# Kernel tuning notes

Measured on AMD Instinct MI355X. Metric: run time of the kernel, lower is better.

## Reference

```python
import math
import jax, jax.numpy as jnp
import numpy as np

HIDDEN = 1024
HEADS = 16
HEAD = HIDDEN // HEADS
BUCKET = 32
MAXPOS = 512
REL = 2 * BUCKET - 1
EPS = 1e-7
L, B = 512, 16
STD = math.sqrt(2.0 / (5.0 * HIDDEN))


def _ln(x, g=None, b=None):
    m = x.mean(-1, keepdims=True)
    v = ((x - m) ** 2).mean(-1, keepdims=True)
    y = (x - m) * jax.lax.rsqrt(v + EPS)
    return y if g is None else y * g + b


def _bucket_indices(n):
    # DeBERTa-style log bucket relative positions, shifted to [0, 2*BUCKET-2]
    r = jnp.arange(n)[:, None] - jnp.arange(n)[None, :]
    mid = BUCKET // 2
    abs_pos = jnp.where((r < mid) & (r > -mid), mid - 1,
                        jnp.clip(jnp.abs(r), None, MAXPOS - 1))
    log_pos = jnp.ceil(jnp.log(abs_pos.astype(jnp.float32) / mid)
                       / math.log((MAXPOS - 1) / mid) * (mid - 1)).astype(jnp.int32) + mid
    bucket_pos = jnp.where(abs_pos <= mid, r, log_pos * jnp.sign(r))
    return (BUCKET - 1 + bucket_pos).astype(jnp.int32)


def setup_inputs() -> dict:
    key = jax.random.key(0)
    ks = jax.random.split(key, 8)
    return {
        'hidden_states': jax.random.normal(ks[0], (L, B, HIDDEN), jnp.float32),
        'attention_mask': jax.random.randint(ks[1], (B, 1, 1, L), 0, 2).astype(bool),
        'relative_embedding': jax.random.normal(ks[2], (REL, HIDDEN), jnp.float32),
        'wqk': jax.random.normal(ks[3], (2 * HIDDEN, HIDDEN), jnp.float32) * STD,
        'bqk': jnp.zeros((2 * HIDDEN,), jnp.float32),
        'wv': jax.random.normal(ks[4], (HIDDEN, HIDDEN), jnp.float32) * STD,
        'bv': jnp.zeros((HIDDEN,), jnp.float32),
        'wo': jax.random.normal(ks[5], (HIDDEN, HIDDEN), jnp.float32) * STD,
        'bo': jnp.zeros((HIDDEN,), jnp.float32),
        'ln_g': jnp.ones((HIDDEN,), jnp.float32),
        'ln_b': jnp.zeros((HIDDEN,), jnp.float32),
    }


def reference(hidden_states, attention_mask, relative_embedding,
              wqk, bqk, wv, bv, wo, bo, ln_g, ln_b):
    Lq, Bq, D = hidden_states.shape
    scale = 1.0 / math.sqrt(3 * HEAD)
    h = _ln(hidden_states)                                 # pre LN, no affine
    q, k = jnp.split(h @ wqk.T + bqk, 2, axis=-1)
    v = h @ wv.T + bv
    qpos, kpos = jnp.split(relative_embedding @ wqk.T + bqk, 2, axis=-1)
    qpos = qpos.reshape(REL, HEADS, HEAD)
    kpos = kpos.reshape(REL, HEADS, HEAD)
    # (L,B,D) -> (B,H,L,hd)
    qh = q.reshape(Lq, Bq, HEADS, HEAD).transpose(1, 2, 0, 3)
    kh = k.reshape(Lq, Bq, HEADS, HEAD).transpose(1, 2, 0, 3)
    vh = v.reshape(Lq, Bq, HEADS, HEAD).transpose(1, 2, 0, 3)
    scores = jnp.einsum('bhqd,bhkd->bhqk', qh, kh) * scale       # c2c
    qp = jnp.einsum('bhqd,khd->bhqk', qh, kpos) * scale          # c2p (k over buckets)
    pk = jnp.einsum('bhkd,qhd->bhqk', kh, qpos) * scale          # p2c (q over buckets)
    idx = jnp.broadcast_to(_bucket_indices(Lq), (Bq, HEADS, Lq, Lq))
    scores = scores + jnp.take_along_axis(qp, idx, axis=-1) \
                    + jnp.take_along_axis(pk, idx, axis=-2)
    # masked softmax: mask==True -> -inf before softmax, 0 after
    probs = jax.nn.softmax(jnp.where(attention_mask, -1e9, scores), axis=-1)
    probs = jnp.where(attention_mask, 0.0, probs)
    ctx = jnp.einsum('bhqk,bhkd->bhqd', probs, vh)
    ctx = ctx.transpose(2, 0, 1, 3).reshape(Lq, Bq, D)           # (L,B,D)
    out = ctx @ wo.T + bo
    return _ln(out, ln_g, ln_b)
```

## Files before the change

### kernel.cpp

```cpp
#include <hip/hip_runtime.h>
#include <hip/hip_bf16.h>

#define HID 1024
#define HEADS 16
#define HEAD 64
#define RELN 63
#define SEQ 512
#define BATCH 16
#define NROWS (SEQ*BATCH)
#define MEXT 8320
#define NQKV 3072
#define LNEPS 1e-7f
#define SCALE2 (0.07216878364870323f * 1.4426950408889634f)

typedef __attribute__((ext_vector_type(4))) float  f32x4;
typedef __attribute__((ext_vector_type(8))) short  s16x8;
typedef __attribute__((ext_vector_type(4))) ushort u16x4;

static __device__ __forceinline__ ushort f2bf(float f) {
  union { float f; unsigned u; } v; v.f = f;
  unsigned r = v.u + 0x7fffu + ((v.u >> 16) & 1u);
  return (ushort)(r >> 16);
}
static __device__ __forceinline__ float bf2f(ushort u) {
  union { unsigned u; float f; } v; v.u = ((unsigned)u) << 16;
  return v.f;
}

__global__ void k_prep(const void* mask_raw, const float* bqk, const float* bv,
                       ushort* mask01, int* idx_tab, float* bcat) {
  __shared__ int s_isbool;
  int tid = threadIdx.x;
  if (tid == 0) s_isbool = 0;
  __syncthreads();
  const unsigned* mu = (const unsigned*)mask_raw;
  int bad = 0;
  for (int i = tid; i < 2048; i += 256) if (mu[i] > 1u) bad = 1;
  if (bad) s_isbool = 1;
  __syncthreads();
  int isbool = s_isbool;
  const unsigned char* m8 = (const unsigned char*)mask_raw;
  const int* m32 = (const int*)mask_raw;
  for (int i = tid; i < BATCH*SEQ; i += 256) {
    int m = isbool ? (int)m8[i] : m32[i];
    mask01[i] = m ? 1 : 0;
  }
  for (int i = tid; i < 1023; i += 256) {
    int r = i - 511;
    int a = r < 0 ? -r : r;
    int absp = (a < 16) ? 15 : (a < 511 ? a : 511);
    int idx;
    if (absp <= 16) idx = 31 + r;
    else {
      float v = logf((float)absp / 16.0f) / logf(511.0f / 16.0f) * 15.0f;
      int lp = (int)ceilf(v) + 16;
      idx = 31 + (r > 0 ? lp : -lp);
    }
    idx_tab[i] = idx;
  }
  for (int i = tid; i < 2048; i += 256) bcat[i] = bqk[i];
  for (int i = tid; i < 1024; i += 256) bcat[2048 + i] = bv[i];
}

__global__ __launch_bounds__(256) void k_convert(const float* wqk, const float* wv, const float* wo,
                                                 ushort* wcat, ushort* wo_b) {
  int c = blockIdx.x * 256 + threadIdx.x;
  f32x4 x; ushort* dst;
  if (c < 524288)      { x = *(const f32x4*)(wqk + (size_t)c * 4);            dst = wcat + (size_t)c * 4; }
  else if (c < 786432) { x = *(const f32x4*)(wv  + (size_t)(c - 524288) * 4); dst = wcat + (size_t)c * 4; }
  else                 { x = *(const f32x4*)(wo  + (size_t)(c - 786432) * 4); dst = wo_b + (size_t)(c - 786432) * 4; }
  u16x4 o = { f2bf(x[0]), f2bf(x[1]), f2bf(x[2]), f2bf(x[3]) };
  *(u16x4*)dst = o;
}

__global__ __launch_bounds__(256) void k_ln1(const float* hid, const float* rel, ushort* h_ext) {
  int row = blockIdx.x, tid = threadIdx.x;
  __shared__ float red[8];
  if (row < NROWS) {
    const float* src = hid + (size_t)row * HID;
    f32x4 x = *(const f32x4*)(src + tid * 4);
    float s = x[0] + x[1] + x[2] + x[3];
    #pragma unroll
    for (int m = 1; m < 64; m <<= 1) s += __shfl_xor(s, m);
    if ((tid & 63) == 0) red[tid >> 6] = s;
    __syncthreads();
    float mean = (red[0] + red[1] + red[2] + red[3]) * (1.0f / HID);
    float d0 = x[0] - mean, d1 = x[1] - mean, d2 = x[2] - mean, d3 = x[3] - mean;
    float sq = d0*d0 + d1*d1 + d2*d2 + d3*d3;
    #pragma unroll
    for (int m = 1; m < 64; m <<= 1) sq += __shfl_xor(sq, m);
    __syncthreads();
    if ((tid & 63) == 0) red[4 + (tid >> 6)] = sq;
    __syncthreads();
    float var = (red[4] + red[5] + red[6] + red[7]) * (1.0f / HID);
    float rs = rsqrtf(var + LNEPS);
    u16x4 o = { f2bf(d0*rs), f2bf(d1*rs), f2bf(d2*rs), f2bf(d3*rs) };
    *(u16x4*)(h_ext + (size_t)row * HID + tid * 4) = o;
  } else if (row < NROWS + RELN) {
    const float* src = rel + (size_t)(row - NROWS) * HID;
    f32x4 x = *(const f32x4*)(src + tid * 4);
    u16x4 o = { f2bf(x[0]), f2bf(x[1]), f2bf(x[2]), f2bf(x[3]) };
    *(u16x4*)(h_ext + (size_t)row * HID + tid * 4) = o;
  } else {
    u16x4 z = { 0, 0, 0, 0 };
    *(u16x4*)(h_ext + (size_t)row * HID + tid * 4) = z;
  }
}

__global__ __launch_bounds__(512) void k_gemm256(const ushort* A, const ushort* Bw, const float* bias,
                                                 ushort* Cb, int M, int N, int K) {
  __shared__ char smem[49152];
  char* As = smem;
  char* Bs = smem + 32768;
  int tid = threadIdx.x, lane = tid & 63, w = tid >> 6;
  int nbn = N >> 7;
  int per = gridDim.x >> 3;
  int gl = (blockIdx.x & 7) * per + (blockIdx.x >> 3);
  int bm = gl / nbn, bn = gl % nbn;
  int wr = w >> 1, wc = w & 1;
  int g = lane >> 4, r = lane & 15;
  f32x4 acc[4][4] = {};
  for (int ko = 0; ko < K; ko += 64) {
    __syncthreads();
    #pragma unroll
    for (int c = 0; c < 4; ++c) {
      int chunk = c * 512 + tid;
      int row = chunk >> 3;
      int kbs = ((chunk & 7) << 4) ^ ((row & 7) << 4);
      int ar = bm * 256 + row; ar = ar < M ? ar : M - 1;
      const char* gA = (const char*)(A + (size_t)ar * K + ko) + kbs;
      __builtin_amdgcn_global_load_lds((const __attribute__((address_space(1))) void*)gA,
                                       (__attribute__((address_space(3))) void*)(As + c * 8192 + w * 1024),
                                       16, 0, 0);
    }
    #pragma unroll
    for (int c = 0; c < 2; ++c) {
      int chunk = c * 512 + tid;
      int row = chunk >> 3;
      int kbs = ((chunk & 7) << 4) ^ ((row & 7) << 4);
      const char* gB = (const char*)(Bw + (size_t)(bn * 128 + row) * K + ko) + kbs;
      __builtin_amdgcn_global_load_lds((const __attribute__((address_space(1))) void*)gB,
                                       (__attribute__((address_space(3))) void*)(Bs + c * 8192 + w * 1024),
                                       16, 0, 0);
    }
    __syncthreads();
    #pragma unroll
    for (int kk = 0; kk < 2; ++kk) {
      s16x8 af[4], bf[4];
      #pragma unroll
      for (int mt = 0; mt < 4; ++mt) {
        int row = wr * 64 + mt * 16 + r;
        int kb = (kk * 64 + g * 16) ^ ((row & 7) << 4);
        af[mt] = *(const s16x8*)(As + row * 128 + kb);
      }
      #pragma unroll
      for (int nt = 0; nt < 4; ++nt) {
        int row = wc * 64 + nt * 16 + r;
        int kb = (kk * 64 + g * 16) ^ ((row & 7) << 4);
        bf[nt] = *(const s16x8*)(Bs + row * 128 + kb);
      }
      #pragma unroll
      for (int mt = 0; mt < 4; ++mt)
        #pragma unroll
        for (int nt = 0; nt < 4; ++nt)
          acc[mt][nt] = __builtin_amdgcn_mfma_f32_16x16x32_bf16(af[mt], bf[nt], acc[mt][nt], 0, 0, 0);
    }
  }
  #pragma unroll
  for (int nt = 0; nt < 4; ++nt) {
    int col = bn * 128 + wc * 64 + nt * 16 + r;
    float bvv = bias[col];
    #pragma unroll
    for (int mt = 0; mt < 4; ++mt) {
      int row0 = bm * 256 + wr * 64 + mt * 16 + g * 4;
      #pragma unroll
      for (int i = 0; i < 4; ++i) {
        int row = row0 + i;
        if (row < M) Cb[(size_t)row * N + col] = f2bf(acc[mt][nt][i] + bvv);
      }
    }
  }
}

__global__ __launch_bounds__(256) void k_gemm_sk(const ushort* A, const ushort* Bw, const float* bias,
                                                 ushort* C0, ushort* C1) {
  const int N = 1024, K = 1024;
  __shared__ char smem[32768];
  char* As = smem;
  char* Bs = smem + 16384;
  int tid = threadIdx.x, lane = tid & 63, w = tid >> 6;
  int per = gridDim.x >> 3;
  int gl = (blockIdx.x & 7) * per + (blockIdx.x >> 3);
  int bn = gl & 7, ks = (gl >> 3) & 1, bm = gl >> 4;
  int wr = w >> 1, wc = w & 1;
  int g = lane >> 4, r = lane & 15;
  f32x4 acc[4][4] = {};
  for (int ko = ks * 512; ko < ks * 512 + 512; ko += 64) {
    __syncthreads();
    #pragma unroll
    for (int c = 0; c < 4; ++c) {
      int chunk = c * 256 + tid;
      int row = chunk >> 3;
      int kbs = ((chunk & 7) << 4) ^ ((row & 7) << 4);
      const char* gA = (const char*)(A + (size_t)(bm * 128 + row) * K + ko) + kbs;
      const char* gB = (const char*)(Bw + (size_t)(bn * 128 + row) * K + ko) + kbs;
      __builtin_amdgcn_global_load_lds((const __attribute__((address_space(1))) void*)gA,
                                       (__attribute__((address_space(3))) void*)(As + c * 4096 + w * 1024),
                                       16, 0, 0);
      __builtin_amdgcn_global_load_lds((const __attribute__((address_space(1))) void*)gB,
                                       (__attribute__((address_space(3))) void*)(Bs + c * 4096 + w * 1024),
                                       16, 0, 0);
    }
    __syncthreads();
    #pragma unroll
    for (int kk = 0; kk < 2; ++kk) {
      s16x8 af[4], bf[4];
      #pragma unroll
      for (int mt = 0; mt < 4; ++mt) {
        int row = wr * 64 + mt * 16 + r;
        int kb = (kk * 64 + g * 16) ^ ((row & 7) << 4);
        af[mt] = *(const s16x8*)(As + row * 128 + kb);
      }
      #pragma unroll
      for (int nt = 0; nt < 4; ++nt) {
        int row = wc * 64 + nt * 16 + r;
        int kb = (kk * 64 + g * 16) ^ ((row & 7) << 4);
        bf[nt] = *(const s16x8*)(Bs + row * 128 + kb);
      }
      #pragma unroll
      for (int mt = 0; mt < 4; ++mt)
        #pragma unroll
        for (int nt = 0; nt < 4; ++nt)
          acc[mt][nt] = __builtin_amdgcn_mfma_f32_16x16x32_bf16(af[mt], bf[nt], acc[mt][nt], 0, 0, 0);
    }
  }
  ushort* C = ks ? C1 : C0;
  #pragma unroll
  for (int nt = 0; nt < 4; ++nt) {
    int col = bn * 128 + wc * 64 + nt * 16 + r;
    float bvv = ks ? 0.0f : bias[col];
    #pragma unroll
    for (int mt = 0; mt < 4; ++mt) {
      int row0 = bm * 128 + wr * 64 + mt * 16 + g * 4;
      #pragma unroll
      for (int i = 0; i < 4; ++i)
        C[(size_t)(row0 + i) * N + col] = f2bf(acc[mt][nt][i] + bvv);
    }
  }
}

__global__ __launch_bounds__(256) void k_pos(const ushort* qkv, const ushort* mask01,
                                             ushort* qp, ushort* pk) {
  int bh = blockIdx.x;
  int b = bh >> 4, h = bh & 15;
  int tid = threadIdx.x, lane = tid & 63, w = tid >> 6;
  int g = lane >> 4, r = lane & 15;
  __shared__ ushort mb[512];
  for (int i = tid; i < 512; i += 256) mb[i] = mask01[b * SEQ + i];
  __syncthreads();
  s16x8 bkp[4][2], bqp[4][2];
  #pragma unroll
  for (int nt = 0; nt < 4; ++nt)
    #pragma unroll
    for (int kk = 0; kk < 2; ++kk) {
      size_t rowp = (size_t)(NROWS + nt * 16 + r);
      int colq = h * 64 + kk * 32 + g * 8;
      bqp[nt][kk] = *(const s16x8*)(qkv + rowp * NQKV + colq);
      bkp[nt][kk] = *(const s16x8*)(qkv + rowp * NQKV + 1024 + colq);
    }
  for (int cc = 0; cc < 8; ++cc) {
    int rowbase = cc * 64 + w * 16;
    s16x8 aq[2], ak[2];
    #pragma unroll
    for (int kk = 0; kk < 2; ++kk) {
      size_t rowq = (size_t)((rowbase + r) * 16 + b);
      int colq = h * 64 + kk * 32 + g * 8;
      aq[kk] = *(const s16x8*)(qkv + rowq * NQKV + colq);
      ak[kk] = *(const s16x8*)(qkv + rowq * NQKV + 1024 + colq);
    }
    f32x4 accq[4] = {}, acck[4] = {};
    #pragma unroll
    for (int kk = 0; kk < 2; ++kk)
      #pragma unroll
      for (int nt = 0; nt < 4; ++nt) {
        accq[nt] = __builtin_amdgcn_mfma_f32_16x16x32_bf16(aq[kk], bkp[nt][kk], accq[nt], 0, 0, 0);
        acck[nt] = __builtin_amdgcn_mfma_f32_16x16x32_bf16(ak[kk], bqp[nt][kk], acck[nt], 0, 0, 0);
      }
    #pragma unroll
    for (int nt = 0; nt < 4; ++nt)
      #pragma unroll
      for (int i = 0; i < 4; ++i) {
        int q = rowbase + g * 4 + i;
        int t = nt * 16 + r;
        float biasv = mb[q] ? -1e9f : 0.0f;
        qp[(size_t)bh * SEQ * 64 + q * 64 + t] = f2bf(accq[nt][i] * SCALE2);
        pk[(size_t)bh * SEQ * 64 + q * 64 + t] = f2bf(acck[nt][i] * SCALE2 + biasv);
      }
  }
}

__global__ __launch_bounds__(256) void k_vt(const ushort* qkv, ushort* vt, ushort* kc) {
  int bid = blockIdx.x;
  int bh = bid >> 3, lt = bid & 7;
  int b = bh >> 4, h = bh & 15;
  __shared__ ushort tile[64][72];
  int tid = threadIdx.x;
  #pragma unroll
  for (int c = 0; c < 2; ++c) {
    int e = (c * 256 + tid) * 8;
    int l = e >> 6, d0 = e & 63;
    size_t row = (size_t)((lt * 64 + l) * 16 + b);
    s16x8 kv = *(const s16x8*)(qkv + row * NQKV + 1024 + h * 64 + d0);
    #pragma unroll
    for (int j = 0; j < 8; ++j) kv[j] = (short)f2bf(bf2f((ushort)kv[j]) * SCALE2);
    *(s16x8*)(kc + ((size_t)bh * SEQ + lt * 64 + l) * 64 + d0) = kv;
    *(s16x8*)&tile[l][d0] = *(const s16x8*)(qkv + row * NQKV + 2048 + h * 64 + d0);
  }
  __syncthreads();
  #pragma unroll
  for (int c = 0; c < 2; ++c) {
    int e = (c * 256 + tid) * 8;
    int d = e >> 6, l0 = e & 63;
    ushort tmp[8];
    #pragma unroll
    for (int j = 0; j < 8; ++j) tmp[j] = tile[l0 + j][d];
    *(s16x8*)(vt + (size_t)(bh * 64 + d) * SEQ + lt * 64 + l0) = *(s16x8*)tmp;
  }
}

__global__ __launch_bounds__(512) void k_attn(const ushort* qkv, const ushort* qp_all, const ushort* pk_all,
                                              const ushort* kc, const ushort* vt,
                                              const int* idx_tab, ushort* ctx) {
  int bid = blockIdx.x;
  int slot = bid >> 3;
  int bh = (bid & 7) * 32 + (slot >> 1);
  int qh = slot & 1;
  int b = bh >> 4, h = bh & 15;
  int tid = threadIdx.x, lane = tid & 63, w = tid >> 6;
  int g = lane >> 4, r = lane & 15;

  __shared__ ushort pk_f[512][68];
  __shared__ ushort qp_s[256][68];
  __shared__ ushort p_s[8][16][68];
  __shared__ ushort idx_s[1024];

  const ushort* qpsrc = qp_all + (size_t)bh * SEQ * 64 + (size_t)qh * 256 * 64;
  const ushort* pksrc = pk_all + (size_t)bh * SEQ * 64;
  const char*   kcb   = (const char*)(kc + (size_t)bh * SEQ * 64);

  #pragma unroll
  for (int c = 0; c < 4; ++c) {
    int chunk = c * 512 + tid;
    int row = chunk >> 3, col8 = (chunk & 7) * 8;
    s16x8 v = *(const s16x8*)(qpsrc + (size_t)row * 64 + col8);
    u16x4 lo = { (ushort)v[0], (ushort)v[1], (ushort)v[2], (ushort)v[3] };
    u16x4 hi = { (ushort)v[4], (ushort)v[5], (ushort)v[6], (ushort)v[7] };
    *(u16x4*)&qp_s[row][col8] = lo;
    *(u16x4*)&qp_s[row][col8 + 4] = hi;
  }
  #pragma unroll
  for (int c = 0; c < 8; ++c) {
    int chunk = c * 512 + tid;
    int row = chunk >> 3, col8 = (chunk & 7) * 8;
    s16x8 v = *(const s16x8*)(pksrc + (size_t)row * 64 + col8);
    u16x4 lo = { (ushort)v[0], (ushort)v[1], (ushort)v[2], (ushort)v[3] };
    u16x4 hi = { (ushort)v[4], (ushort)v[5], (ushort)v[6], (ushort)v[7] };
    *(u16x4*)&pk_f[row][col8] = lo;
    *(u16x4*)&pk_f[row][col8 + 4] = hi;
  }
  for (int i = tid; i < 1023; i += 512) idx_s[i] = (ushort)idx_tab[i];
  s16x8 aq[2][2];
  #pragma unroll
  for (int qs = 0; qs < 2; ++qs)
    #pragma unroll
    for (int kk = 0; kk < 2; ++kk) {
      int qglob = qh * 256 + qs * 128 + w * 16 + r;
      aq[qs][kk] = *(const s16x8*)(qkv + ((size_t)qglob * 16 + b) * NQKV + h * 64 + kk * 32 + g * 8);
    }
  __syncthreads();

  float m_i[2] = { -3e38f, -3e38f }, l_i[2] = { 0.0f, 0.0f };
  f32x4 o_acc[2][4] = {};

  for (int kt = 0; kt < 8; ++kt) {
    s16x8 kf[4][2], vf[2][4];
    #pragma unroll
    for (int nt = 0; nt < 4; ++nt)
      #pragma unroll
      for (int kk = 0; kk < 2; ++kk)
        kf[nt][kk] = *(const s16x8*)(kcb + (size_t)(kt * 64 + nt * 16 + r) * 128 + kk * 64 + g * 16);
    #pragma unroll
    for (int kk = 0; kk < 2; ++kk)
      #pragma unroll
      for (int nt = 0; nt < 4; ++nt)
        vf[kk][nt] = *(const s16x8*)(vt + (size_t)(bh * 64 + nt * 16 + r) * SEQ + kt * 64 + kk * 32 + g * 8);

    #pragma unroll
    for (int qs = 0; qs < 2; ++qs) {
      f32x4 s[4];
      #pragma unroll
      for (int nt = 0; nt < 4; ++nt) {
        f32x4 a = {};
        #pragma unroll
        for (int kk = 0; kk < 2; ++kk)
          a = __builtin_amdgcn_mfma_f32_16x16x32_bf16(kf[nt][kk], aq[qs][kk], a, 0, 0, 0);
        s[nt] = a;
      }

      const ushort* qprow = &qp_s[qs * 128 + w * 16 + r][0];
      const int qg511 = qh * 256 + qs * 128 + w * 16 + r + 511;
      float m_loc = -3e38f;
      #pragma unroll
      for (int nt = 0; nt < 4; ++nt) {
        #pragma unroll
        for (int i = 0; i < 4; ++i) {
          int kg = kt * 64 + nt * 16 + g * 4 + i;
          int t = idx_s[qg511 - kg];
          float v = s[nt][i] + bf2f(qprow[t]) + bf2f(pk_f[kg][t]);
          s[nt][i] = v;
          m_loc = fmaxf(m_loc, v);
        }
      }

      float mx = fmaxf(m_loc, __shfl_xor(m_loc, 16));
      mx = fmaxf(mx, __shfl_xor(mx, 32));

      if (__any(mx > m_i[qs] + 8.0f)) {
        float mnew = fmaxf(m_i[qs], mx);
        float rs = exp2f(m_i[qs] - mnew);
        m_i[qs] = mnew;
        l_i[qs] *= rs;
        float rsb[4];
        #pragma unroll
        for (int i = 0; i < 4; ++i) rsb[i] = __shfl(rs, g * 4 + i);
        #pragma unroll
        for (int nt = 0; nt < 4; ++nt)
          #pragma unroll
          for (int i = 0; i < 4; ++i) o_acc[qs][nt][i] *= rsb[i];
      }

      float psum = 0.0f;
      #pragma unroll
      for (int nt = 0; nt < 4; ++nt) {
        u16x4 pk4;
        #pragma unroll
        for (int i = 0; i < 4; ++i) {
          float pe = exp2f(s[nt][i] - m_i[qs]);
          psum += pe;
          pk4[i] = f2bf(pe);
        }
        *(u16x4*)&p_s[w][r][nt * 16 + g * 4] = pk4;
      }
      psum += __shfl_xor(psum, 16);
      psum += __shfl_xor(psum, 32);
      l_i[qs] += psum;

      #pragma unroll
      for (int kk = 0; kk < 2; ++kk) {
        u16x4 lo = *(const u16x4*)&p_s[w][r][kk * 32 + g * 8];
        u16x4 hi = *(const u16x4*)&p_s[w][r][kk * 32 + g * 8 + 4];
        s16x8 pa = { (short)lo[0], (short)lo[1], (short)lo[2], (short)lo[3],
                     (short)hi[0], (short)hi[1], (short)hi[2], (short)hi[3] };
        #pragma unroll
        for (int nt = 0; nt < 4; ++nt)
          o_acc[qs][nt] = __builtin_amdgcn_mfma_f32_16x16x32_bf16(pa, vf[kk][nt], o_acc[qs][nt], 0, 0, 0);
      }
    }
  }

  #pragma unroll
  for (int qs = 0; qs < 2; ++qs) {
    float lb[4];
    #pragma unroll
    for (int i = 0; i < 4; ++i) lb[i] = __shfl(l_i[qs], g * 4 + i);
    #pragma unroll
    for (int i = 0; i < 4; ++i) {
      float inv = lb[i] > 0.0f ? 1.0f / lb[i] : 0.0f;
      int lq = qh * 256 + qs * 128 + w * 16 + g * 4 + i;
      size_t rowc = (size_t)(lq * 16 + b);
      #pragma unroll
      for (int nt = 0; nt < 4; ++nt)
        ctx[rowc * HID + h * 64 + nt * 16 + r] = f2bf(o_acc[qs][nt][i] * inv);
    }
  }
}

__global__ __launch_bounds__(256) void k_ln2(const ushort* t0, const ushort* t1,
                                             const float* gamma, const float* beta, float* out) {
  int row = blockIdx.x, tid = threadIdx.x;
  __shared__ float red[8];
  u16x4 xa = *(const u16x4*)(t0 + (size_t)row * HID + tid * 4);
  u16x4 xb = *(const u16x4*)(t1 + (size_t)row * HID + tid * 4);
  float x[4];
  #pragma unroll
  for (int j = 0; j < 4; ++j) x[j] = bf2f(xa[j]) + bf2f(xb[j]);
  float s = x[0] + x[1] + x[2] + x[3];
  #pragma unroll
  for (int m = 1; m < 64; m <<= 1) s += __shfl_xor(s, m);
  if ((tid & 63) == 0) red[tid >> 6] = s;
  __syncthreads();
  float mean = (red[0] + red[1] + red[2] + red[3]) * (1.0f / HID);
  float d[4]; float sq = 0.0f;
  #pragma unroll
  for (int j = 0; j < 4; ++j) { d[j] = x[j] - mean; sq += d[j] * d[j]; }
  #pragma unroll
  for (int m = 1; m < 64; m <<= 1) sq += __shfl_xor(sq, m);
  __syncthreads();
  if ((tid & 63) == 0) red[4 + (tid >> 6)] = sq;
  __syncthreads();
  float var = (red[4] + red[5] + red[6] + red[7]) * (1.0f / HID);
  float rs = rsqrtf(var + LNEPS);
  f32x4 o;
  #pragma unroll
  for (int j = 0; j < 4; ++j) o[j] = d[j] * rs * gamma[tid * 4 + j] + beta[tid * 4 + j];
  *(f32x4*)(out + (size_t)row * HID + tid * 4) = o;
}

extern "C" void kernel_launch(void* const* d_in, const int* in_sizes, int n_in,
                              void* d_out, int out_size, void* d_ws, size_t ws_size,
                              hipStream_t stream) {
  (void)in_sizes; (void)n_in; (void)out_size; (void)ws_size;
  const float* hid  = (const float*)d_in[0];
  const void*  mask = d_in[1];
  const float* rel  = (const float*)d_in[2];
  const float* wqk  = (const float*)d_in[3];
  const float* bqk  = (const float*)d_in[4];
  const float* wv   = (const float*)d_in[5];
  const float* bv   = (const float*)d_in[6];
  const float* wo   = (const float*)d_in[7];
  const float* bo   = (const float*)d_in[8];
  const float* ln_g = (const float*)d_in[9];
  const float* ln_b = (const float*)d_in[10];

  char* ws = (char*)d_ws;
  ushort* wcat     = (ushort*)(ws);
  ushort* wo_b     = (ushort*)(ws + 6291456);
  float*  bcat     = (float*) (ws + 8388608);
  ushort* mask01   = (ushort*)(ws + 8400896);
  int*    idx_tab  = (int*)   (ws + 8433664);
  ushort* h_ext    = (ushort*)(ws + 8437760);
  ushort* qkv      = (ushort*)(ws + 25477120);
  ushort* qp_b     = (ushort*)(ws + 76595200);
  ushort* pk_b     = (ushort*)(ws + 93372416);
  ushort* vt       = (ushort*)(ws + 110149632);
  char*   tmpr     = (ws + 126926848);
  ushort* ctx = h_ext;
  ushort* kc   = (ushort*)tmpr;
  ushort* tmp0 = (ushort*)tmpr;
  ushort* tmp1 = (ushort*)(tmpr + 16777216);

  k_prep<<<1, 256, 0, stream>>>(mask, bqk, bv, mask01, idx_tab, bcat);
  k_convert<<<4096, 256, 0, stream>>>(wqk, wv, wo, wcat, wo_b);
  k_ln1<<<MEXT, 256, 0, stream>>>(hid, rel, h_ext);
  k_gemm256<<<33 * (NQKV / 128), 512, 0, stream>>>(h_ext, wcat, bcat, qkv, MEXT, NQKV, 1024);
  k_pos<<<256, 256, 0, stream>>>(qkv, mask01, qp_b, pk_b);
  k_vt<<<2048, 256, 0, stream>>>(qkv, vt, kc);
  k_attn<<<512, 512, 0, stream>>>(qkv, qp_b, pk_b, kc, vt, idx_tab, ctx);
  k_gemm_sk<<<1024, 256, 0, stream>>>(ctx, wo_b, bo, tmp0, tmp1);
  k_ln2<<<NROWS, 256, 0, stream>>>(tmp0, tmp1, ln_g, ln_b, (float*)d_out);
}
```

Measured before the change: 255.1 us.

## Fold QK scale into GEMM epilogue, read pk from global, add setprio

Moves the softmax scale for Q and K into the QKV GEMM epilogue, so it is dropped from the positional kernel and from the K copy kernel. The attention kernel no longer stages the full 512x64 pk table in LDS and gathers pk directly from global memory/L2, which cuts LDS use and may raise occupancy. It also pads p_s so the P fragment can be read as one 16-byte load, brackets the MFMA blocks with s_setprio, and uses the HIP bf16 conversion intrinsic. The risk is that scattered global gathers for pk add latency to the inner loop. Applying the scale before rounding to bf16 also slightly changes numerics.

```diff
diff --git a/kernel.cpp b/kernel.cpp
--- a/kernel.cpp
+++ b/kernel.cpp
@@ -18,9 +18,8 @@
 typedef __attribute__((ext_vector_type(4))) ushort u16x4;
 
 static __device__ __forceinline__ ushort f2bf(float f) {
-  union { float f; unsigned u; } v; v.f = f;
-  unsigned r = v.u + 0x7fffu + ((v.u >> 16) & 1u);
-  return (ushort)(r >> 16);
+  __hip_bfloat16 h = __float2bfloat16(f);
+  return *reinterpret_cast<ushort*>(&h);
 }
 static __device__ __forceinline__ float bf2f(ushort u) {
   union { unsigned u; float f; } v; v.u = ((unsigned)u) << 16;
@@ -170,13 +169,14 @@
   for (int nt = 0; nt < 4; ++nt) {
     int col = bn * 128 + wc * 64 + nt * 16 + r;
     float bvv = bias[col];
+    float sc = (col < 1024) ? SCALE2 : 1.0f;
     #pragma unroll
     for (int mt = 0; mt < 4; ++mt) {
       int row0 = bm * 256 + wr * 64 + mt * 16 + g * 4;
       #pragma unroll
       for (int i = 0; i < 4; ++i) {
         int row = row0 + i;
-        if (row < M) Cb[(size_t)row * N + col] = f2bf(acc[mt][nt][i] + bvv);
+        if (row < M) Cb[(size_t)row * N + col] = f2bf((acc[mt][nt][i] + bvv) * sc);
       }
     }
   }
@@ -293,8 +293,8 @@
         int q = rowbase + g * 4 + i;
         int t = nt * 16 + r;
         float biasv = mb[q] ? -1e9f : 0.0f;
-        qp[(size_t)bh * SEQ * 64 + q * 64 + t] = f2bf(accq[nt][i] * SCALE2);
-        pk[(size_t)bh * SEQ * 64 + q * 64 + t] = f2bf(acck[nt][i] * SCALE2 + biasv);
+        qp[(size_t)bh * SEQ * 64 + q * 64 + t] = f2bf(accq[nt][i]);
+        pk[(size_t)bh * SEQ * 64 + q * 64 + t] = f2bf(acck[nt][i] + biasv);
       }
   }
 }
@@ -311,8 +311,6 @@
     int l = e >> 6, d0 = e & 63;
     size_t row = (size_t)((lt * 64 + l) * 16 + b);
     s16x8 kv = *(const s16x8*)(qkv + row * NQKV + 1024 + h * 64 + d0);
-    #pragma unroll
-    for (int j = 0; j < 8; ++j) kv[j] = (short)f2bf(bf2f((ushort)kv[j]) * SCALE2);
     *(s16x8*)(kc + ((size_t)bh * SEQ + lt * 64 + l) * 64 + d0) = kv;
     *(s16x8*)&tile[l][d0] = *(const s16x8*)(qkv + row * NQKV + 2048 + h * 64 + d0);
   }
@@ -339,13 +337,12 @@
   int tid = threadIdx.x, lane = tid & 63, w = tid >> 6;
   int g = lane >> 4, r = lane & 15;
 
-  __shared__ ushort pk_f[512][68];
   __shared__ ushort qp_s[256][68];
-  __shared__ ushort p_s[8][16][68];
+  __shared__ ushort p_s[8][16][72];
   __shared__ ushort idx_s[1024];
 
   const ushort* qpsrc = qp_all + (size_t)bh * SEQ * 64 + (size_t)qh * 256 * 64;
-  const ushort* pksrc = pk_all + (size_t)bh * SEQ * 64;
+  const ushort* pkbh  = pk_all + (size_t)bh * SEQ * 64;
   const char*   kcb   = (const char*)(kc + (size_t)bh * SEQ * 64);
 
   #pragma unroll
@@ -358,16 +355,6 @@
     *(u16x4*)&qp_s[row][col8] = lo;
     *(u16x4*)&qp_s[row][col8 + 4] = hi;
   }
-  #pragma unroll
-  for (int c = 0; c < 8; ++c) {
-    int chunk = c * 512 + tid;
-    int row = chunk >> 3, col8 = (chunk & 7) * 8;
-    s16x8 v = *(const s16x8*)(pksrc + (size_t)row * 64 + col8);
-    u16x4 lo = { (ushort)v[0], (ushort)v[1], (ushort)v[2], (ushort)v[3] };
-    u16x4 hi = { (ushort)v[4], (ushort)v[5], (ushort)v[6], (ushort)v[7] };
-    *(u16x4*)&pk_f[row][col8] = lo;
-    *(u16x4*)&pk_f[row][col8 + 4] = hi;
-  }
   for (int i = tid; i < 1023; i += 512) idx_s[i] = (ushort)idx_tab[i];
   s16x8 aq[2][2];
   #pragma unroll
@@ -398,6 +385,7 @@
     #pragma unroll
     for (int qs = 0; qs < 2; ++qs) {
       f32x4 s[4];
+      __builtin_amdgcn_s_setprio(1);
       #pragma unroll
       for (int nt = 0; nt < 4; ++nt) {
         f32x4 a = {};
@@ -406,6 +394,7 @@
           a = __builtin_amdgcn_mfma_f32_16x16x32_bf16(kf[nt][kk], aq[qs][kk], a, 0, 0, 0);
         s[nt] = a;
       }
+      __builtin_amdgcn_s_setprio(0);
 
       const ushort* qprow = &qp_s[qs * 128 + w * 16 + r][0];
       const int qg511 = qh * 256 + qs * 128 + w * 16 + r + 511;
@@ -416,7 +405,7 @@
         for (int i = 0; i < 4; ++i) {
           int kg = kt * 64 + nt * 16 + g * 4 + i;
           int t = idx_s[qg511 - kg];
-          float v = s[nt][i] + bf2f(qprow[t]) + bf2f(pk_f[kg][t]);
+          float v = s[nt][i] + bf2f(qprow[t]) + bf2f(pkbh[kg * 64 + t]);
           s[nt][i] = v;
           m_loc = fmaxf(m_loc, v);
         }
@@ -455,16 +444,15 @@
       psum += __shfl_xor(psum, 32);
       l_i[qs] += psum;
 
+      __builtin_amdgcn_s_setprio(1);
       #pragma unroll
       for (int kk = 0; kk < 2; ++kk) {
-        u16x4 lo = *(const u16x4*)&p_s[w][r][kk * 32 + g * 8];
-        u16x4 hi = *(const u16x4*)&p_s[w][r][kk * 32 + g * 8 + 4];
-        s16x8 pa = { (short)lo[0], (short)lo[1], (short)lo[2], (short)lo[3],
-                     (short)hi[0], (short)hi[1], (short)hi[2], (short)hi[3] };
+        s16x8 pa = *(const s16x8*)&p_s[w][r][kk * 32 + g * 8];
         #pragma unroll
         for (int nt = 0; nt < 4; ++nt)
           o_acc[qs][nt] = __builtin_amdgcn_mfma_f32_16x16x32_bf16(pa, vf[kk][nt], o_acc[qs][nt], 0, 0, 0);
       }
+      __builtin_amdgcn_s_setprio(0);
     }
   }
 
```

Result: slower. 296.3 us (+16.2%).
